# Performance work log

Hardware: AMD Instinct MI355X
Metric: run time of the kernel (lower is better)

Reference implementation:

```python
import jax, jax.numpy as jnp
import numpy as np

B, S, D = 1, 2048, 4096
N_HEADS, N_KV_HEADS = 32, 8
HEAD_DIM = D // N_HEADS  # 128


def setup_inputs() -> dict:
    key = jax.random.key(0)
    ks = jax.random.split(key, 6)
    x = jax.random.normal(ks[0], (B, S, D), dtype=jnp.float32)
    # weights stored as [in, out] so forward is x @ W (== torch x @ W.T with W [out,in])
    sc = 0.02
    wq = jax.random.normal(ks[1], (D, N_HEADS * HEAD_DIM), dtype=jnp.float32) * sc
    wk = jax.random.normal(ks[2], (D, N_KV_HEADS * HEAD_DIM), dtype=jnp.float32) * sc
    wv = jax.random.normal(ks[3], (D, N_KV_HEADS * HEAD_DIM), dtype=jnp.float32) * sc
    wo = jax.random.normal(ks[4], (N_HEADS * HEAD_DIM, D), dtype=jnp.float32) * sc
    # rotary tables: freqs_cis as cos/sin of shape [S, HEAD_DIM//2]
    inv_freq = 1.0 / (10000.0 ** (np.arange(0, HEAD_DIM, 2, dtype=np.float32) / HEAD_DIM))
    t = np.arange(S, dtype=np.float32)
    freqs = np.outer(t, inv_freq)  # [S, HEAD_DIM//2]
    cos = jnp.asarray(np.cos(freqs), dtype=jnp.float32)
    sin = jnp.asarray(np.sin(freqs), dtype=jnp.float32)
    # additive causal mask [S, S]: 0 on/below diagonal, -inf above
    mask = jnp.where(jnp.tril(jnp.ones((S, S), dtype=bool)), 0.0, -1e9).astype(jnp.float32)
    return {"x": x, "wq": wq, "wk": wk, "wv": wv, "wo": wo,
            "cos": cos, "sin": sin, "mask": mask}


def _apply_rope(t, cos, sin):
    # t: [B, S, H, Hd]; interpret last dim as Hd//2 complex pairs (interleaved)
    b, s, h, hd = t.shape
    tr = t.reshape(b, s, h, hd // 2, 2)
    t1, t2 = tr[..., 0], tr[..., 1]
    c = cos[None, :, None, :]  # [1, S, 1, Hd//2]
    sn = sin[None, :, None, :]
    o1 = t1 * c - t2 * sn
    o2 = t1 * sn + t2 * c
    return jnp.stack([o1, o2], axis=-1).reshape(b, s, h, hd)


def reference(x, wq, wk, wv, wo, cos, sin, mask):
    b, s, d = x.shape
    hd = 2 * cos.shape[-1]
    nh = wq.shape[1] // hd
    nkv = wk.shape[1] // hd
    n_rep = nh // nkv
    q = (x @ wq).reshape(b, s, nh, hd)
    k = (x @ wk).reshape(b, s, nkv, hd)
    v = (x @ wv).reshape(b, s, nkv, hd)
    q = _apply_rope(q, cos, sin)
    k = _apply_rope(k, cos, sin)
    # repeat_kv along head dim
    k = jnp.repeat(k, n_rep, axis=2)  # [B, S, H, Hd]
    v = jnp.repeat(v, n_rep, axis=2)
    scale = 1.0 / jnp.sqrt(jnp.float32(hd))
    scores = jnp.einsum('bqhd,bkhd->bhqk', q, k) * scale + mask[None, None, :, :]
    probs = jax.nn.softmax(scores, axis=-1)
    out = jnp.einsum('bhqk,bkhd->bqhd', probs, v).reshape(b, s, nh * hd)
    return out @ wo
```

## Files before the change

### kernel.cpp

```cpp
#include <hip/hip_runtime.h>
#include <hip/hip_bf16.h>

typedef unsigned short u16;
typedef unsigned int   u32;
typedef __attribute__((ext_vector_type(8))) short bf16x8;
typedef __attribute__((ext_vector_type(4))) short bf16x4;
typedef __attribute__((ext_vector_type(4))) float f32x4;
typedef __attribute__((ext_vector_type(4))) unsigned short u16x4;

__device__ __forceinline__ u16 f32_to_bf16bits(float f) {
    u32 x = __float_as_uint(f);
    u32 r = (x + 0x7fffu + ((x >> 16) & 1u)) >> 16;
    return (u16)r;
}
__device__ __forceinline__ float bf16bits_to_f32(u16 u) {
    return __uint_as_float(((u32)u) << 16);
}
__device__ __forceinline__ u32 cvt_pk_bf16(float lo, float hi) {
    u32 r;
    asm("v_cvt_pk_bf16_f32 %0, %1, %2" : "=v"(r) : "v"(lo), "v"(hi));
    return r;
}

__device__ __forceinline__ void async_copy16(void* lds, const void* g) {
    __builtin_amdgcn_global_load_lds(
        (__attribute__((address_space(1))) void*)(g),
        (__attribute__((address_space(3))) void*)(lds), 16, 0, 0);
}

__global__ void convert_f32_bf16(const float* __restrict__ src, u16* __restrict__ dst, int n4) {
    const int i = blockIdx.x * 256 + threadIdx.x;
    if (i >= n4) return;
    const float4 v = ((const float4*)src)[i];
    u16x4 o = { f32_to_bf16bits(v.x), f32_to_bf16bits(v.y),
                f32_to_bf16bits(v.z), f32_to_bf16bits(v.w) };
    ((u16x4*)dst)[i] = o;
}

__global__ void transpose_wT(const float* __restrict__ src, u16* __restrict__ dst,
                             int N, int dstStride) {
    __shared__ float tile[32][33];
    const int n0 = blockIdx.x * 32, k0 = blockIdx.y * 32;
    const int tx = threadIdx.x, ty = threadIdx.y;
#pragma unroll
    for (int i = 0; i < 4; ++i)
        tile[ty + i*8][tx] = src[(size_t)(k0 + ty + i*8) * N + n0 + tx];
    __syncthreads();
#pragma unroll
    for (int i = 0; i < 4; ++i)
        dst[(size_t)(n0 + ty + i*8) * dstStride + k0 + tx] =
            f32_to_bf16bits(tile[tx][ty + i*8]);
}

__global__ void transpose_v(const u16* __restrict__ qkv, u16* __restrict__ vT) {
    __shared__ u16 tile[32][34];
    const int s0 = blockIdx.x * 32, n0 = blockIdx.y * 32;
    const int tx = threadIdx.x, ty = threadIdx.y;
#pragma unroll
    for (int i = 0; i < 4; ++i)
        tile[ty + i*8][tx] = qkv[(size_t)(s0 + ty + i*8) * 6144 + 5120 + n0 + tx];
    __syncthreads();
#pragma unroll
    for (int i = 0; i < 4; ++i)
        vT[(size_t)(n0 + ty + i*8) * 2048 + s0 + tx] = tile[tx][ty + i*8];
}

__global__ void rope_kernel(u32* __restrict__ qkv, const float* __restrict__ cosp,
                            const float* __restrict__ sinp) {
    const int s = blockIdx.x;
    const int h = blockIdx.y * 4 + (threadIdx.x >> 6);
    const int p = threadIdx.x & 63;
    const size_t off = ((size_t)s * 6144 + h * 128) >> 1;
    const u32 packed = qkv[off + p];
    const float c  = cosp[s*64 + p], sn = sinp[s*64 + p];
    const float t1 = bf16bits_to_f32((u16)(packed & 0xffffu));
    const float t2 = bf16bits_to_f32((u16)(packed >> 16));
    const float o1 = t1 * c - t2 * sn;
    const float o2 = t1 * sn + t2 * c;
    qkv[off + p] = (u32)f32_to_bf16bits(o1) | ((u32)f32_to_bf16bits(o2) << 16);
}

template<bool BF16OUT>
__global__ __launch_bounds__(256, 2) void gemm_bt(
    const u16* __restrict__ A, const u16* __restrict__ B, void* __restrict__ Cv,
    int N, int K) {
    __shared__ __align__(16) char sm[32768];
    char* sA = sm;
    char* sB = sm + 16384;
    const int tid = threadIdx.x;
    const int w = tid >> 6, l = tid & 63;
    const int wm = w >> 1, wn = w & 1;
    const int bm = blockIdx.y, bn = blockIdx.x;
    const int g = l >> 4, c0 = l & 15;

    f32x4 acc[4][4] = {};

    const int srow   = w*8 + (l >> 3);
    const int schunk = (l & 7) ^ (l >> 3);
    const u16* Ab = A + (size_t)(bm*128 + srow) * K + schunk * 8;
    const u16* Bb = B + (size_t)(bn*128 + srow) * K + schunk * 8;

    const int nkt = K >> 6;
    for (int kt = 0; kt < nkt; ++kt) {
        const int kofs = kt * 64;
#pragma unroll
        for (int i = 0; i < 4; ++i) {
            async_copy16(sA + (i*32 + w*8) * 128, Ab + (size_t)(i*32) * K + kofs);
            async_copy16(sB + (i*32 + w*8) * 128, Bb + (size_t)(i*32) * K + kofs);
        }
        __syncthreads();
#pragma unroll
        for (int dks = 0; dks < 2; ++dks) {
            bf16x8 af[4], bfr[4];
            const int chunk = (dks*4 + g) ^ (l & 7);
#pragma unroll
            for (int i = 0; i < 4; ++i) {
                af[i]  = *(const bf16x8*)(sA + (wm*64 + i*16 + c0) * 128 + chunk * 16);
                bfr[i] = *(const bf16x8*)(sB + (wn*64 + i*16 + c0) * 128 + chunk * 16);
            }
#pragma unroll
            for (int i = 0; i < 4; ++i)
#pragma unroll
                for (int j = 0; j < 4; ++j)
                    acc[i][j] = __builtin_amdgcn_mfma_f32_16x16x32_bf16(
                        af[i], bfr[j], acc[i][j], 0, 0, 0);
        }
        __syncthreads();
    }

#pragma unroll
    for (int i = 0; i < 4; ++i)
#pragma unroll
        for (int j = 0; j < 4; ++j) {
            const int row = bm*128 + wm*64 + i*16 + g*4;
            const int col = bn*128 + wn*64 + j*16 + c0;
#pragma unroll
            for (int r = 0; r < 4; ++r) {
                if (BF16OUT)
                    ((u16*)Cv)[(size_t)(row + r) * N + col] = f32_to_bf16bits(acc[i][j][r]);
                else
                    ((float*)Cv)[(size_t)(row + r) * N + col] = acc[i][j][r];
            }
        }
}

__global__ __launch_bounds__(256, 2) void attn_kernel(
    const u16* __restrict__ qkv, const u16* __restrict__ vT, u16* __restrict__ outp) {
    __shared__ __align__(16) char lds[65536];
    const int tid = threadIdx.x;
    const int w = tid >> 6, l = tid & 63;
    const int g = l >> 4, c0 = l & 15;
    const int qt = (blockIdx.y < 16) ? blockIdx.x : (15 - (int)blockIdx.x);
    const int h = blockIdx.y;
    const int kvh = h >> 2;
    const int q0g = qt * 128;
    const int qrow0 = q0g + w * 32;

    const int srK = w*4 + g,        scK = c0 ^ srK;
    const int srV = w*8 + (l >> 3), scV = (l & 7) ^ (l >> 3);

#pragma unroll
    for (int i = 0; i < 8; ++i)
        async_copy16(lds + (i*16 + w*4) * 256,
                     qkv + (size_t)(q0g + i*16 + srK) * 6144 + h*128 + scK*8);
    __syncthreads();

#pragma unroll
    for (int i = 0; i < 4; ++i)
        async_copy16(lds + 32768 + (i*16 + w*4) * 256,
                     qkv + (size_t)(i*16 + srK) * 6144 + 4096 + kvh*128 + scK*8);
#pragma unroll
    for (int i = 0; i < 4; ++i)
        async_copy16(lds + 49152 + (i*32 + w*8) * 128,
                     vT + (size_t)(kvh*128 + i*32 + srV) * 2048 + scV*8);

    bf16x8 qf[2][4];
#pragma unroll
    for (int i = 0; i < 2; ++i)
#pragma unroll
        for (int dks = 0; dks < 4; ++dks) {
            const int row = w*32 + i*16 + c0;
            qf[i][dks] = *(const bf16x8*)(lds + row*256 + (((dks*4 + g) ^ c0) * 16));
        }
    __syncthreads();

    f32x4 o[2][8] = {};
    float lsum[2] = {0.f, 0.f};
    const int ntiles = 2*qt + 2;
    const float SC2 = 0.08838834764831845f * 1.4426950408889634f;

    for (int kt = 0; kt < ntiles; ++kt) {
        const int cur = kt & 1;
        const char* kb = lds + (cur ? 0 : 32768);
        const char* vb = lds + (cur ? 16384 : 49152);
        if (kt + 1 < ntiles) {
            char* kbn = lds + ((cur ^ 1) ? 0 : 32768);
            char* vbn = lds + ((cur ^ 1) ? 16384 : 49152);
#pragma unroll
            for (int i = 0; i < 4; ++i)
                async_copy16(kbn + (i*16 + w*4) * 256,
                             qkv + (size_t)((kt+1)*64 + i*16 + srK) * 6144 + 4096 + kvh*128 + scK*8);
#pragma unroll
            for (int i = 0; i < 4; ++i)
                async_copy16(vbn + (i*32 + w*8) * 128,
                             vT + (size_t)(kvh*128 + i*32 + srV) * 2048 + (kt+1)*64 + scV*8);
        }

        if (kt*64 <= qrow0 + 31) {
            f32x4 st[2][4] = {};
            __builtin_amdgcn_s_setprio(1);
#pragma unroll
            for (int dks = 0; dks < 4; ++dks) {
                bf16x8 kf[4];
#pragma unroll
                for (int j = 0; j < 4; ++j) {
                    const int row = j*16 + c0;
                    kf[j] = *(const bf16x8*)(kb + row*256 + (((dks*4 + g) ^ c0) * 16));
                }
#pragma unroll
                for (int i = 0; i < 2; ++i)
#pragma unroll
                    for (int j = 0; j < 4; ++j)
                        st[i][j] = __builtin_amdgcn_mfma_f32_16x16x32_bf16(
                            kf[j], qf[i][dks], st[i][j], 0, 0, 0);
            }
            __builtin_amdgcn_s_setprio(0);

            const bool diag = (kt*64 + 63) > qrow0;
            u32 pk[2][4][2];
#pragma unroll
            for (int i = 0; i < 2; ++i) {
                float rowsum = 0.f;
#pragma unroll
                for (int j = 0; j < 4; ++j) {
#pragma unroll
                    for (int r = 0; r < 4; ++r) {
                        float p = exp2f(st[i][j][r] * SC2);
                        if (diag) {
                            const int kgl = kt*64 + j*16 + g*4 + r;
                            const int qgl = qrow0 + i*16 + c0;
                            if (kgl > qgl) p = 0.f;
                        }
                        st[i][j][r] = p;
                        rowsum += p;
                    }
                    pk[i][j][0] = cvt_pk_bf16(st[i][j][0], st[i][j][1]);
                    pk[i][j][1] = cvt_pk_bf16(st[i][j][2], st[i][j][3]);
                }
                rowsum += __shfl_xor(rowsum, 16);
                rowsum += __shfl_xor(rowsum, 32);
                lsum[i] += rowsum;
            }

#pragma unroll
            for (int dks = 0; dks < 2; ++dks) {
                bf16x8 pf[2];
#pragma unroll
                for (int i = 0; i < 2; ++i) {
                    union { u32 u[4]; bf16x8 v; } pu;
                    pu.u[0] = pk[i][2*dks][0];   pu.u[1] = pk[i][2*dks][1];
                    pu.u[2] = pk[i][2*dks+1][0]; pu.u[3] = pk[i][2*dks+1][1];
                    pf[i] = pu.v;
                }
                __builtin_amdgcn_s_setprio(1);
#pragma unroll
                for (int dj = 0; dj < 8; ++dj) {
                    const int row = dj*16 + c0;
                    const int cg0 = (4*dks + (g >> 1)) ^ (row & 7);
                    const int cg1 = (4*dks + (g >> 1) + 2) ^ (row & 7);
                    union { struct { bf16x4 lo, hi; } p; bf16x8 v; } vu;
                    vu.p.lo = *(const bf16x4*)(vb + row*128 + cg0*16 + 8*(g & 1));
                    vu.p.hi = *(const bf16x4*)(vb + row*128 + cg1*16 + 8*(g & 1));
#pragma unroll
                    for (int i = 0; i < 2; ++i)
                        o[i][dj] = __builtin_amdgcn_mfma_f32_16x16x32_bf16(
                            vu.v, pf[i], o[i][dj], 0, 0, 0);
                }
                __builtin_amdgcn_s_setprio(0);
            }
        }
        __syncthreads();
    }

#pragma unroll
    for (int i = 0; i < 2; ++i) {
        const float rcp = 1.0f / lsum[i];
        const int qg = qrow0 + i*16 + c0;
#pragma unroll
        for (int dj = 0; dj < 8; ++dj) {
            u16x4 ov = { f32_to_bf16bits(o[i][dj][0] * rcp),
                         f32_to_bf16bits(o[i][dj][1] * rcp),
                         f32_to_bf16bits(o[i][dj][2] * rcp),
                         f32_to_bf16bits(o[i][dj][3] * rcp) };
            *(u16x4*)(outp + (size_t)qg * 4096 + h*128 + dj*16 + g*4) = ov;
        }
    }
}

extern "C" void kernel_launch(void* const* d_in, const int* in_sizes, int n_in,
                              void* d_out, int out_size, void* d_ws, size_t ws_size,
                              hipStream_t stream) {
    const float* x    = (const float*)d_in[0];
    const float* wq   = (const float*)d_in[1];
    const float* wk   = (const float*)d_in[2];
    const float* wv   = (const float*)d_in[3];
    const float* wo   = (const float*)d_in[4];
    const float* cosp = (const float*)d_in[5];
    const float* sinp = (const float*)d_in[6];

    char* ws = (char*)d_ws;
    u16* xb    = (u16*)(ws);
    u16* wqkvT = (u16*)(ws + 16777216);
    u16* woT   = (u16*)(ws + 67108864);
    u16* qkv   = (u16*)(ws + 100663296);
    u16* vTb   = (u16*)(ws + 125829120);
    u16* attn  = (u16*)(ws + 130023424);

    dim3 tb(32, 8);
    convert_f32_bf16<<<8192, 256, 0, stream>>>(x, xb, 2097152);
    transpose_wT<<<dim3(128, 128), tb, 0, stream>>>(wq, wqkvT, 4096, 4096);
    transpose_wT<<<dim3(32, 128),  tb, 0, stream>>>(wk, wqkvT + (size_t)4096*4096, 1024, 4096);
    transpose_wT<<<dim3(32, 128),  tb, 0, stream>>>(wv, wqkvT + (size_t)5120*4096, 1024, 4096);
    transpose_wT<<<dim3(128, 128), tb, 0, stream>>>(wo, woT, 4096, 4096);

    gemm_bt<true><<<dim3(48, 16), 256, 0, stream>>>(xb, wqkvT, qkv, 6144, 4096);
    rope_kernel<<<dim3(2048, 10), 256, 0, stream>>>((u32*)qkv, cosp, sinp);
    transpose_v<<<dim3(64, 32), tb, 0, stream>>>(qkv, vTb);
    attn_kernel<<<dim3(16, 32), 256, 0, stream>>>(qkv, vTb, attn);
    gemm_bt<false><<<dim3(32, 16), 256, 0, stream>>>(attn, woT, d_out, 4096, 4096);
}
```

Baseline: 328.2 us.

## Replace GEMMs with 4-slot ring-buffered 512-thread kernel and widen weight transpose

Replaces the synchronous 128x128 GEMM with a 512-thread kernel using 256-wide N tiles, a 4-slot LDS ring with two-stage-ahead async global-to-LDS loads, partial vmcnt waits, a single barrier per k-step and raised wave priority around MFMAs. It also restructures the weight transpose to process 128 columns per block and write packed 32-bit bf16 pairs. The aim is to hide load latency and cut barriers and transpose store inefficiency. It risks more register pressure and lower occupancy from the larger LDS footprint, and the hand-tuned vmcnt counts must match the number of issued loads.

```diff
diff --git a/kernel.cpp b/kernel.cpp
--- a/kernel.cpp
+++ b/kernel.cpp
@@ -39,17 +39,24 @@
 
 __global__ void transpose_wT(const float* __restrict__ src, u16* __restrict__ dst,
                              int N, int dstStride) {
-    __shared__ float tile[32][33];
-    const int n0 = blockIdx.x * 32, k0 = blockIdx.y * 32;
+    __shared__ float tile[32][129];
+    const int n0 = blockIdx.x * 128, k0 = blockIdx.y * 32;
     const int tx = threadIdx.x, ty = threadIdx.y;
 #pragma unroll
-    for (int i = 0; i < 4; ++i)
-        tile[ty + i*8][tx] = src[(size_t)(k0 + ty + i*8) * N + n0 + tx];
+    for (int j = 0; j < 4; ++j)
+#pragma unroll
+        for (int i = 0; i < 4; ++i)
+            tile[ty + 8*j][tx + 32*i] = src[(size_t)(k0 + ty + 8*j) * N + n0 + tx + 32*i];
     __syncthreads();
-#pragma unroll
-    for (int i = 0; i < 4; ++i)
-        dst[(size_t)(n0 + ty + i*8) * dstStride + k0 + tx] =
-            f32_to_bf16bits(tile[tx][ty + i*8]);
+    const int tid = ty * 32 + tx;
+    const int c = tid & 15, nl0 = tid >> 4;
+#pragma unroll
+    for (int s = 0; s < 8; ++s) {
+        const int nl = nl0 + s * 16;
+        const u32 pk = (u32)f32_to_bf16bits(tile[2*c][nl])
+                     | ((u32)f32_to_bf16bits(tile[2*c + 1][nl]) << 16);
+        *(u32*)&dst[(size_t)(n0 + nl) * dstStride + k0 + 2*c] = pk;
+    }
 }
 
 __global__ void transpose_v(const u16* __restrict__ qkv, u16* __restrict__ vT) {
@@ -80,66 +87,90 @@
     qkv[off + p] = (u32)f32_to_bf16bits(o1) | ((u32)f32_to_bf16bits(o2) << 16);
 }
 
-template<bool BF16OUT>
-__global__ __launch_bounds__(256, 2) void gemm_bt(
+template<int MFRAG, bool BF16OUT>
+__global__ __launch_bounds__(512, 2) void gemm_ring(
     const u16* __restrict__ A, const u16* __restrict__ B, void* __restrict__ Cv,
-    int N, int K) {
-    __shared__ __align__(16) char sm[32768];
-    char* sA = sm;
-    char* sB = sm + 16384;
+    int N, int K, int nbn) {
+    constexpr int BM     = MFRAG * 32;
+    constexpr int ABYTES = BM * 64;
+    constexpr int SLOT   = ABYTES + 16384;
+    __shared__ __align__(16) char sm[4 * SLOT];
+
     const int tid = threadIdx.x;
     const int w = tid >> 6, l = tid & 63;
-    const int wm = w >> 1, wn = w & 1;
-    const int bm = blockIdx.y, bn = blockIdx.x;
+    const int wm = w >> 2, wn = w & 3;
     const int g = l >> 4, c0 = l & 15;
-
-    f32x4 acc[4][4] = {};
-
-    const int srow   = w*8 + (l >> 3);
-    const int schunk = (l & 7) ^ (l >> 3);
-    const u16* Ab = A + (size_t)(bm*128 + srow) * K + schunk * 8;
-    const u16* Bb = B + (size_t)(bn*128 + srow) * K + schunk * 8;
-
-    const int nkt = K >> 6;
+    const int bid = blockIdx.x;
+    const int bm = bid / nbn, bn = bid % nbn;
+
+    const int srow   = l >> 2;
+    const int schunk = (l & 3) ^ (srow & 3) ^ ((srow >> 2) & 3);
+    const u16* As = A + (size_t)(bm * BM  + w*16 + srow) * K + schunk * 8;
+    const u16* Bs = B + (size_t)(bn * 256 + w*16 + srow) * K + schunk * 8;
+
+    const int rswz = ((g ^ (c0 & 3) ^ ((c0 >> 2) & 3)) & 3) * 16;
+
+    f32x4 acc[MFRAG][4] = {};
+
+    auto stage = [&](int st, int ss) {
+        char* aB = sm + ss * SLOT;
+        char* bB = aB + ABYTES;
+        const u16* as = As + (size_t)st * 32;
+        const u16* bs = Bs + (size_t)st * 32;
+        async_copy16(aB + (w*16) * 64, as);
+        if (MFRAG == 8)
+            async_copy16(aB + (128 + w*16) * 64, as + (size_t)128 * K);
+        async_copy16(bB + (w*16) * 64, bs);
+        async_copy16(bB + (128 + w*16) * 64, bs + (size_t)128 * K);
+    };
+
+    const int nkt = K >> 5;
+    stage(0, 0);
+    stage(1, 1);
+
     for (int kt = 0; kt < nkt; ++kt) {
-        const int kofs = kt * 64;
-#pragma unroll
-        for (int i = 0; i < 4; ++i) {
-            async_copy16(sA + (i*32 + w*8) * 128, Ab + (size_t)(i*32) * K + kofs);
-            async_copy16(sB + (i*32 + w*8) * 128, Bb + (size_t)(i*32) * K + kofs);
-        }
-        __syncthreads();
-#pragma unroll
-        for (int dks = 0; dks < 2; ++dks) {
-            bf16x8 af[4], bfr[4];
-            const int chunk = (dks*4 + g) ^ (l & 7);
-#pragma unroll
-            for (int i = 0; i < 4; ++i) {
-                af[i]  = *(const bf16x8*)(sA + (wm*64 + i*16 + c0) * 128 + chunk * 16);
-                bfr[i] = *(const bf16x8*)(sB + (wn*64 + i*16 + c0) * 128 + chunk * 16);
-            }
-#pragma unroll
-            for (int i = 0; i < 4; ++i)
-#pragma unroll
-                for (int j = 0; j < 4; ++j)
-                    acc[i][j] = __builtin_amdgcn_mfma_f32_16x16x32_bf16(
-                        af[i], bfr[j], acc[i][j], 0, 0, 0);
-        }
-        __syncthreads();
+        const int st = (kt + 2 < nkt) ? kt + 2 : nkt - 1;
+        stage(st, (kt + 2) & 3);
+        if (MFRAG == 8) asm volatile("s_waitcnt vmcnt(8)" ::: "memory");
+        else            asm volatile("s_waitcnt vmcnt(6)" ::: "memory");
+        __builtin_amdgcn_s_barrier();
+        asm volatile("" ::: "memory");
+
+        const char* aB = sm + (kt & 3) * SLOT;
+        const char* bB = aB + ABYTES;
+        bf16x8 bfr[4];
+#pragma unroll
+        for (int n = 0; n < 4; ++n)
+            bfr[n] = *(const bf16x8*)(bB + (wn*64 + n*16 + c0) * 64 + rswz);
+        bf16x8 afr[MFRAG];
+#pragma unroll
+        for (int m = 0; m < MFRAG; ++m)
+            afr[m] = *(const bf16x8*)(aB + (wm*(BM/2) + m*16 + c0) * 64 + rswz);
+
+        __builtin_amdgcn_s_setprio(1);
+#pragma unroll
+        for (int m = 0; m < MFRAG; ++m)
+#pragma unroll
+            for (int n = 0; n < 4; ++n)
+                acc[m][n] = __builtin_amdgcn_mfma_f32_16x16x32_bf16(
+                    afr[m], bfr[n], acc[m][n], 0, 0, 0);
+        __builtin_amdgcn_s_setprio(0);
+        asm volatile("" ::: "memory");
     }
-
-#pragma unroll
-    for (int i = 0; i < 4; ++i)
-#pragma unroll
-        for (int j = 0; j < 4; ++j) {
-            const int row = bm*128 + wm*64 + i*16 + g*4;
-            const int col = bn*128 + wn*64 + j*16 + c0;
+    asm volatile("s_waitcnt vmcnt(0)" ::: "memory");
+
+#pragma unroll
+    for (int m = 0; m < MFRAG; ++m)
+#pragma unroll
+        for (int n = 0; n < 4; ++n) {
+            const int row = bm*BM + wm*(BM/2) + m*16 + g*4;
+            const int col = bn*256 + wn*64 + n*16 + c0;
 #pragma unroll
             for (int r = 0; r < 4; ++r) {
                 if (BF16OUT)
-                    ((u16*)Cv)[(size_t)(row + r) * N + col] = f32_to_bf16bits(acc[i][j][r]);
+                    ((u16*)Cv)[(size_t)(row + r) * N + col] = f32_to_bf16bits(acc[m][n][r]);
                 else
-                    ((float*)Cv)[(size_t)(row + r) * N + col] = acc[i][j][r];
+                    ((float*)Cv)[(size_t)(row + r) * N + col] = acc[m][n][r];
             }
         }
 }
@@ -318,14 +349,14 @@
 
     dim3 tb(32, 8);
     convert_f32_bf16<<<8192, 256, 0, stream>>>(x, xb, 2097152);
-    transpose_wT<<<dim3(128, 128), tb, 0, stream>>>(wq, wqkvT, 4096, 4096);
-    transpose_wT<<<dim3(32, 128),  tb, 0, stream>>>(wk, wqkvT + (size_t)4096*4096, 1024, 4096);
-    transpose_wT<<<dim3(32, 128),  tb, 0, stream>>>(wv, wqkvT + (size_t)5120*4096, 1024, 4096);
-    transpose_wT<<<dim3(128, 128), tb, 0, stream>>>(wo, woT, 4096, 4096);
-
-    gemm_bt<true><<<dim3(48, 16), 256, 0, stream>>>(xb, wqkvT, qkv, 6144, 4096);
+    transpose_wT<<<dim3(32, 128), tb, 0, stream>>>(wq, wqkvT, 4096, 4096);
+    transpose_wT<<<dim3(8, 128),  tb, 0, stream>>>(wk, wqkvT + (size_t)4096*4096, 1024, 4096);
+    transpose_wT<<<dim3(8, 128),  tb, 0, stream>>>(wv, wqkvT + (size_t)5120*4096, 1024, 4096);
+    transpose_wT<<<dim3(32, 128), tb, 0, stream>>>(wo, woT, 4096, 4096);
+
+    gemm_ring<8, true><<<192, 512, 0, stream>>>(xb, wqkvT, qkv, 6144, 4096, 24);
     rope_kernel<<<dim3(2048, 10), 256, 0, stream>>>((u32*)qkv, cosp, sinp);
     transpose_v<<<dim3(64, 32), tb, 0, stream>>>(qkv, vTb);
     attn_kernel<<<dim3(16, 32), 256, 0, stream>>>(qkv, vTb, attn);
-    gemm_bt<false><<<dim3(32, 16), 256, 0, stream>>>(attn, woT, d_out, 4096, 4096);
-}
+    gemm_ring<4, false><<<256, 512, 0, stream>>>(attn, woT, d_out, 4096, 4096, 16);
+}
```

Result: no change. 330.3 us (+0.6%).
